# Kernel optimization log

Hardware: AMD Instinct MI355X
Metric: run time of the kernel (lower is better)

Reference implementation:

```python
import jax, jax.numpy as jnp
import numpy as np

DIM, QK, GS, DEPTH, VOCAB, ROT = 16, 128, 256, 8, 1024, 32
EPS = 1e-5


def scale_norm(x, g):
    # ScaleNorm: x / max(||x|| * dim^-0.5, eps) * g
    norm = jnp.linalg.norm(x, axis=-1, keepdims=True) * (DIM ** -0.5)
    return x / jnp.clip(norm, EPS) * g


def rotate_half(x):
    # interleaved pairs: (x0,x1,x2,x3,...) -> (-x1,x0,-x3,x2,...)
    xr = x.reshape(x.shape[:-1] + (-1, 2))
    a, b = xr[..., 0], xr[..., 1]
    return jnp.stack((-b, a), axis=-1).reshape(x.shape)


def apply_rotary(x, cos, sin):
    # rotary applied to first ROT dims only
    xr, xp = x[..., :ROT], x[..., ROT:]
    return jnp.concatenate([xr * cos + rotate_half(xr) * sin, xp], axis=-1)


def flash_layer(x, p, cos, sin, keymask, n):
    b = x.shape[0]
    normed = scale_norm(x, p['norm_g'])
    # shift_tokens: first half of channels shifted forward by one position
    xs, xp = jnp.split(normed, 2, axis=-1)
    xs = jnp.pad(xs, ((0, 0), (1, 0), (0, 0)))[:, :-1]
    normed = jnp.concatenate([xs, xp], axis=-1)
    hid = jax.nn.silu(normed @ p['Wh'] + p['bh'])  # [b,n,64]
    v, gate = jnp.split(hid, 2, axis=-1)           # each [b,n,32]
    qk = jax.nn.silu(normed @ p['Wqk'] + p['bqk'])  # [b,n,128]
    offs = qk[..., None, :] * p['gamma'] + p['beta']  # [b,n,4,128]
    quad_q, lin_q, quad_k, lin_k = [apply_rotary(offs[..., i, :], cos, sin) for i in range(4)]
    pad = (-n) % GS
    grp = lambda t: jnp.pad(t, ((0, 0), (0, pad), (0, 0))).reshape(b, -1, GS, t.shape[-1])
    quad_q, quad_k, lin_q, lin_k, vg = map(grp, (quad_q, quad_k, lin_q, lin_k, v))
    # quadratic (local, within-group) attention with ReLU^2
    sim = jnp.einsum('bgid,bgjd->bgij', quad_q, quad_k) / GS
    attn = jnp.square(jax.nn.relu(sim)) * keymask  # mask out padded keys
    quad_out = jnp.einsum('bgij,bgjd->bgid', attn, vg)
    # linear (global, across-group) attention, reduced over groups
    lin_kv = jnp.einsum('bgnd,bgne->bde', lin_k, vg) / n
    lin_out = jnp.einsum('bgnd,bde->bgne', lin_q, lin_kv)
    out = (quad_out + lin_out).reshape(b, -1, v.shape[-1])[:, :n]
    out = gate * out
    return out @ p['Wo'] + p['bo'] + x


def forward(kmer_data, token_emb, pos_scale, norm_g, Wh, bh, Wqk, bqk, gamma, beta, Wo, bo, final_g, Wl, bl, W1, b1, W2, b2):
    b, n = kmer_data.shape
    x = token_emb[kmer_data]  # [b,n,16]
    t = jnp.arange(n, dtype=jnp.float32)
    # ScaledSinuEmbedding
    inv = 1.0 / (10000.0 ** (jnp.arange(0, DIM, 2, dtype=jnp.float32) / DIM))
    sinu = t[:, None] * inv[None, :]
    pos = jnp.concatenate([jnp.sin(sinu), jnp.cos(sinu)], axis=-1) * pos_scale
    x = x + pos
    # rotary tables (dim 32, interleaved repeat)
    rinv = 1.0 / (10000.0 ** (jnp.arange(0, ROT, 2, dtype=jnp.float32) / ROT))
    rf = jnp.repeat(t[:, None] * rinv[None, :], 2, axis=-1)  # [n,32]
    cos, sin = jnp.cos(rf), jnp.sin(rf)
    # key mask for padded positions (996 -> 1024)
    pad = (-n) % GS
    keymask = jnp.pad(jnp.ones((n,), jnp.float32), (0, pad)).reshape(1, -1, 1, GS)
    for i in range(DEPTH):
        p = dict(norm_g=norm_g[i], Wh=Wh[i], bh=bh[i], Wqk=Wqk[i], bqk=bqk[i],
                 gamma=gamma[i], beta=beta[i], Wo=Wo[i], bo=bo[i])
        x = flash_layer(x, p, cos, sin, keymask, n)
    logits = scale_norm(x, final_g) @ Wl + bl  # [b,n,1024]
    h = jnp.max(logits, axis=-1)               # AdaptiveMaxPool1d(1) + Flatten -> [b,n]
    h = jax.nn.relu(h @ W1 + b1)
    return h @ W2 + b2                          # [b,1]


def setup_inputs() -> dict:
    key = jax.random.key(0)
    ks = jax.random.split(key, 12)
    r = lambda k, shape, s: jax.random.normal(k, shape, jnp.float32) * s
    return {
        'kmer_data': jax.random.randint(ks[0], (128, 996), 0, VOCAB),
        'token_emb': r(ks[1], (VOCAB, DIM), 1.0),
        'pos_scale': jnp.float32(1.0),
        'norm_g': jnp.ones((DEPTH,), jnp.float32),
        'Wh': r(ks[2], (DEPTH, DIM, 64), 0.1),
        'bh': jnp.zeros((DEPTH, 64), jnp.float32),
        'Wqk': r(ks[3], (DEPTH, DIM, QK), 0.1),
        'bqk': jnp.zeros((DEPTH, QK), jnp.float32),
        'gamma': 1.0 + r(ks[4], (DEPTH, 4, QK), 0.02),
        'beta': r(ks[5], (DEPTH, 4, QK), 0.02),
        'Wo': r(ks[6], (DEPTH, 32, DIM), 0.1),
        'bo': jnp.zeros((DEPTH, DIM), jnp.float32),
        'final_g': jnp.float32(1.0),
        'Wl': r(ks[7], (DIM, VOCAB), 0.1),
        'bl': jnp.zeros((VOCAB,), jnp.float32),
        'W1': r(ks[8], (996, 32), 0.05),
        'b1': jnp.zeros((32,), jnp.float32),
        'W2': r(ks[9], (32, 1), 0.1),
        'b2': jnp.zeros((1,), jnp.float32),
    }


def reference(kmer_data, token_emb, pos_scale, norm_g, Wh, bh, Wqk, bqk, gamma, beta, Wo, bo, final_g, Wl, bl, W1, b1, W2, b2):
    return forward(kmer_data, token_emb, pos_scale, norm_g, Wh, bh, Wqk, bqk,
                   gamma, beta, Wo, bo, final_g, Wl, bl, W1, b1, W2, b2)
```

## Files before the change

### kernel.cpp

```cpp
#include <hip/hip_runtime.h>

typedef short s16x8 __attribute__((ext_vector_type(8)));
typedef float f32x4 __attribute__((ext_vector_type(4)));

#define NB    128
#define NTOK  996
#define NPAD  1024
#define NGRP  4
#define GSZ   256
#define NLAY  8

__device__ __forceinline__ float bf2f(unsigned short u){
    unsigned int v = ((unsigned int)u) << 16;
    return __uint_as_float(v);
}
__device__ __forceinline__ unsigned short f2bf(float f){
    unsigned int x = __float_as_uint(f);
    unsigned int r = (x + 0x7fffu + ((x >> 16) & 1u)) >> 16;
    return (unsigned short)r;
}
__device__ __forceinline__ unsigned int packbf(float a, float b){
    return (unsigned int)f2bf(a) | ((unsigned int)f2bf(b) << 16);
}
__device__ __forceinline__ float silu(float v){
    return v / (1.0f + __expf(-v));
}

__device__ __forceinline__ void bar_lds(){
    asm volatile("s_waitcnt lgkmcnt(0)\n\ts_barrier" ::: "memory");
}

__device__ __forceinline__ s16x8 derive_core(const unsigned short* __restrict__ qrow, int d0,
        float4 g0, float4 g1, float4 b0, float4 b1,
        const float* __restrict__ rp, bool rot){
    uint4 u = *(const uint4*)(qrow + d0);
    float y0 = bf2f((unsigned short)(u.x & 0xffffu))*g0.x + b0.x;
    float y1 = bf2f((unsigned short)(u.x >> 16))    *g0.y + b0.y;
    float y2 = bf2f((unsigned short)(u.y & 0xffffu))*g0.z + b0.z;
    float y3 = bf2f((unsigned short)(u.y >> 16))    *g0.w + b0.w;
    float y4 = bf2f((unsigned short)(u.z & 0xffffu))*g1.x + b1.x;
    float y5 = bf2f((unsigned short)(u.z >> 16))    *g1.y + b1.y;
    float y6 = bf2f((unsigned short)(u.w & 0xffffu))*g1.z + b1.z;
    float y7 = bf2f((unsigned short)(u.w >> 16))    *g1.w + b1.w;
    if (rot){
        float4 c4 = *(const float4*)(rp);
        float4 s4 = *(const float4*)(rp + 16);
        float a;
        a = y0; y0 = a*c4.x - y1*s4.x; y1 = y1*c4.x + a*s4.x;
        a = y2; y2 = a*c4.y - y3*s4.y; y3 = y3*c4.y + a*s4.y;
        a = y4; y4 = a*c4.z - y5*s4.z; y5 = y5*c4.z + a*s4.z;
        a = y6; y6 = a*c4.w - y7*s4.w; y7 = y7*c4.w + a*s4.w;
    }
    union { unsigned int uu[4]; s16x8 s; } r;
    r.uu[0] = packbf(y0, y1);
    r.uu[1] = packbf(y2, y3);
    r.uu[2] = packbf(y4, y5);
    r.uu[3] = packbf(y6, y7);
    return r.s;
}

__global__ __launch_bounds__(256) void k_embed(const int* __restrict__ kmer,
                                               const float* __restrict__ emb,
                                               const float* __restrict__ ps,
                                               float* __restrict__ x,
                                               float* __restrict__ rope){
    int gid = blockIdx.x * 256 + threadIdx.x;
    if (gid < NPAD){
        float tf2 = (float)gid;
        #pragma unroll
        for (int i = 0; i < 16; i++){
            float inv = expf(((float)(2*i) / 32.0f) * -9.210340371976184f);
            float ang = tf2 * inv;
            rope[gid*32 + i]      = cosf(ang);
            rope[gid*32 + 16 + i] = sinf(ang);
        }
    }
    if (gid >= NB * NTOK) return;
    int b = gid / NTOK;
    int tt = gid - b * NTOK;
    int idx = kmer[gid];
    const float* er = emb + (size_t)idx * 16;
    float pscale = ps[0];
    float tf = (float)tt;
    float* xr = x + (size_t)gid * 16;
    #pragma unroll
    for (int i = 0; i < 8; i++){
        float inv = expf(((float)(2*i) / 16.0f) * -9.210340371976184f);
        float ang = tf * inv;
        xr[i]     = er[i]     + sinf(ang) * pscale;
        xr[8 + i] = er[8 + i] + cosf(ang) * pscale;
    }
}

__global__ __launch_bounds__(512, 2) void k_pre(const float* __restrict__ x,
                                             const float* __restrict__ Wh, const float* __restrict__ bh,
                                             const float* __restrict__ Wqk, const float* __restrict__ bqk,
                                             const float* __restrict__ norm_g,
                                             const float* __restrict__ gamma, const float* __restrict__ beta,
                                             const float* __restrict__ rope, int layer,
                                             unsigned short* __restrict__ qk,
                                             unsigned short* __restrict__ vT,
                                             unsigned short* __restrict__ gateb,
                                             float* __restrict__ linkvp){
    __shared__ __align__(16) unsigned char sm[58880];
    unsigned short* WcT = (unsigned short*)sm;
    unsigned short* As  = (unsigned short*)(sm + 15360);
    unsigned short* LkT = (unsigned short*)(sm + 15360);
    unsigned short* Vt  = (unsigned short*)(sm + 50176);
    int tid = threadIdx.x;
    int qt = blockIdx.x & 3, b = blockIdx.x >> 2;
    const float* Whl = Wh  + (size_t)layer * 1024;
    const float* Wql = Wqk + (size_t)layer * 2048;
    const float* gLin = gamma + (size_t)layer * 512 + 384;
    const float* bLin = beta  + (size_t)layer * 512 + 384;
    for (int i = tid; i < 1024; i += 512){ int d = i >> 6, c2 = i & 63;  WcT[c2*40 + d] = f2bf(Whl[i]); }
    for (int i = tid; i < 2048; i += 512){ int d = i >> 7, c2 = i & 127; WcT[(64 + c2)*40 + d] = f2bf(Wql[i]); }
    if (tid < 192){
        int i = tid;
        float bv = (i < 64) ? bh[layer*64 + i] : bqk[layer*128 + (i - 64)];
        WcT[i*40 + 16] = f2bf(bv);
        WcT[i*40 + 17] = 0;
        unsigned int* zz = (unsigned int*)(WcT + i*40 + 18);
        #pragma unroll
        for (int k = 0; k < 7; k++) zz[k] = 0u;
    }
    float g = norm_g[layer];
    if (tid < 256){
        int tt = qt*256 + tid;
        int tsafe = tt < NTOK ? tt : (NTOK - 1);
        unsigned int* dd = (unsigned int*)(As + tid * 40);
        const float4* xr4 = (const float4*)(x + ((size_t)b*NTOK + tsafe) * 16);
        float cur[16];
        float s2 = 0.f;
        #pragma unroll
        for (int c2 = 0; c2 < 4; c2++){
            float4 v4 = xr4[c2];
// ... 70 lines not shown
                *(uint2*)(gateb + rowq*32 + (wc0 - 32)) = make_uint2(packbf(sv[0],sv[1]), packbf(sv[2],sv[3]));
            } else {
                int qd = wc0 - 64;
                *(uint2*)(qk + rowq*128 + qd) = make_uint2(packbf(sv[0],sv[1]), packbf(sv[2],sv[3]));
                float y0 = sv[0]*gLin[qd]   + bLin[qd];
                float y1 = sv[1]*gLin[qd+1] + bLin[qd+1];
                float y2 = sv[2]*gLin[qd+2] + bLin[qd+2];
                float y3 = sv[3]*gLin[qd+3] + bLin[qd+3];
                if (qd < 32){
                    const float* rp = rope + ttk*32 + (qd >> 1);
                    float c0 = rp[0], s0 = rp[16], c1 = rp[1], s1 = rp[17];
                    float a;
                    a = y0; y0 = a*c0 - y1*s0; y1 = y1*c0 + a*s0;
                    a = y2; y2 = a*c1 - y3*s1; y3 = y3*c1 + a*s1;
                }
                LkT[(qd+0)*136 + c] = f2bf(y0);
                LkT[(qd+1)*136 + c] = f2bf(y1);
                LkT[(qd+2)*136 + c] = f2bf(y2);
                LkT[(qd+3)*136 + c] = f2bf(y3);
            }
        }
        bar_lds();
        #pragma unroll
        for (int ks2 = 0; ks2 < 4; ks2++){
            s16x8 a  = *(const s16x8*)(LkT + (w*16 + m16)*136 + ks2*32 + quad*8);
            s16x8 b0 = *(const s16x8*)(Vt + (m16)*136 + ks2*32 + quad*8);
            s16x8 b1 = *(const s16x8*)(Vt + (16 + m16)*136 + ks2*32 + quad*8);
            lacc[0] = __builtin_amdgcn_mfma_f32_16x16x32_bf16(a, b0, lacc[0], 0,0,0);
            lacc[1] = __builtin_amdgcn_mfma_f32_16x16x32_bf16(a, b1, lacc[1], 0,0,0);
        }
        bar_lds();
    }
    {
        unsigned short* mv = (unsigned short*)sm + w*1280;
        #pragma unroll
        for (int nt = 0; nt < 2; nt++){
            #pragma unroll
            for (int mi = 0; mi < 2; mi++){
                int e0 = mi*16 + quad*4;
                mv[(e0+0)*40 + nt*16 + m16] = (unsigned short)(vpk[nt][mi][0] & 0xffffu);
                mv[(e0+1)*40 + nt*16 + m16] = (unsigned short)(vpk[nt][mi][0] >> 16);
                mv[(e0+2)*40 + nt*16 + m16] = (unsigned short)(vpk[nt][mi][1] & 0xffffu);
                mv[(e0+3)*40 + nt*16 + m16] = (unsigned short)(vpk[nt][mi][1] >> 16);
            }
        }
        #pragma unroll
        for (int r2 = 0; r2 < 2; r2++){
            int e = r2*16 + (lane >> 2);
            int cc = (lane & 3) * 8;
            s16x8 vv = *(const s16x8*)(mv + e*40 + cc);
            *(s16x8*)(vT + ((size_t)b*32 + e)*NPAD + qt*256 + w*32 + cc) = vv;
        }
    }
    {
        float* ml = (float*)(sm + 20480) + w*512;
        const float invn = 1.0f / 996.0f;
        #pragma unroll
        for (int j = 0; j < 2; j++)
            #pragma unroll
            for (int reg = 0; reg < 4; reg++)
                ml[(j*16 + m16)*16 + quad*4 + reg] = lacc[j][reg] * invn;
        #pragma unroll
        for (int r2 = 0; r2 < 2; r2++){
            int e = r2*16 + (lane >> 2);
            int dc = (lane & 3) * 4;
            float4 vv = *(const float4*)(ml + e*16 + dc);
            *(float4*)(linkvp + (((size_t)qt*NB + b)*32 + e)*128 + w*16 + dc) = vv;
        }
    }
}

#define KD_BYTES (64*136*2)
#define PW_BYTES (8*32*72*2)
__global__ __launch_bounds__(512, 2) void k_quad(const unsigned short* __restrict__ qk,
                                              const unsigned short* __restrict__ vT,
                                              const unsigned short* __restrict__ gateb,
                                              const float* __restrict__ linkvp,
                                              const float* __restrict__ rope,
                                              const float* __restrict__ gamma, const float* __restrict__ beta,
                                              int layer,
                                              const float* __restrict__ Wo, const float* __restrict__ bo,
                                              float* __restrict__ x){
    __shared__ __align__(16) unsigned char smem[KD_BYTES + PW_BYTES];
    __shared__ __align__(16) unsigned short LkBs[32 * 136];
    __shared__ float sWo[512];
    __shared__ float sbo[16];
    unsigned short* Kd = (unsigned short*)smem;
    unsigned short* Pw = (unsigned short*)(smem + KD_BYTES);
    int tid = threadIdx.x;
    int blk = blockIdx.x;
    int g = blk & 3, b = blk >> 2;
    int tg0 = g * GSZ;
    const float* gamL = gamma + (size_t)layer * 512;
    const float* betL = beta  + (size_t)layer * 512;
    sWo[tid] = Wo[layer*512 + tid];
    if (tid < 16) sbo[tid] = bo[layer*16 + tid];

    int w = tid >> 6, lane = tid & 63, m16 = lane & 15, quad = lane >> 4;

    int tqA = tg0 + w*32 + m16;
    int tqB = tqA + 16;
    const unsigned short* qrowA = qk + ((size_t)b*NPAD + tqA)*128;
    const unsigned short* qrowB = qk + ((size_t)b*NPAD + tqB)*128;
    const float* rpA = rope + tqA*32 + quad*4;
    const float* rpB = rope + tqB*32 + quad*4;
    s16x8 qf[2][4];
    #pragma unroll
    for (int ks = 0; ks < 4; ks++){
        int d0 = ks*32 + quad*8;
        float4 g0 = *(const float4*)(gamL + d0), g1 = *(const float4*)(gamL + d0 + 4);
        float4 b0 = *(const float4*)(betL + d0), b1 = *(const float4*)(betL + d0 + 4);
        bool rot = (ks == 0) && (quad < 4);
        qf[0][ks] = derive_core(qrowA, d0, g0,g1,b0,b1, rpA, rot);
        qf[1][ks] = derive_core(qrowB, d0, g0,g1,b0,b1, rpB, rot);
    }

    const float* gK = gamL + 256;
    const float* bK = betL + 256;
    f32x4 oacc[2][2] = {{{0,0,0,0},{0,0,0,0}},{{0,0,0,0},{0,0,0,0}}};
    unsigned short* myP = Pw + w*32*72;

    int kr = tid >> 3, seg = (tid & 7) * 16;
    uint4 pku0, pku1;
    float4 prc0, prc1, prs0, prs1;
    auto LOADK = [&](int ch){
        int tk = tg0 + ch*64 + kr;
        const unsigned short* krow = qk + ((size_t)b*NPAD + tk)*128 + seg;
        pku0 = ((const uint4*)krow)[0];
        pku1 = ((const uint4*)krow)[1];
        const float* rpk = rope + (seg < 32 ? (tk*32 + (seg >> 1)) : 0);
        prc0 = *(const float4*)(rpk);
        prs0 = *(const float4*)(rpk + 16);
        prc1 = *(const float4*)(rpk + 4);
        prs1 = *(const float4*)(rpk + 20);
    };
    LOADK(0);

    for (int ch = 0; ch < 4; ch++){
        s16x8 vf[2][2];
        #pragma unroll
        for (int ks2 = 0; ks2 < 2; ks2++){
            vf[ks2][0] = *(const s16x8*)(vT + ((size_t)b*32 + m16)*NPAD + tg0 + ch*64 + ks2*32 + quad*8);
            vf[ks2][1] = *(const s16x8*)(vT + ((size_t)b*32 + 16 + m16)*NPAD + tg0 + ch*64 + ks2*32 + quad*8);
        }
        uint4 kd0, kd1;
        {
            #pragma unroll
            for (int h = 0; h < 2; h++){
                uint4 u = h ? pku1 : pku0;
                unsigned int uu[4] = {u.x, u.y, u.z, u.w};
                float y[8];
                #pragma unroll
                for (int k = 0; k < 4; k++){
                    int d = h*8 + 2*k;
                    y[2*k]   = bf2f((unsigned short)(uu[k] & 0xffffu)) * gK[seg + d]     + bK[seg + d];
                    y[2*k+1] = bf2f((unsigned short)(uu[k] >> 16))     * gK[seg + d + 1] + bK[seg + d + 1];
                }
                if (seg < 32){
                    float cc[4], ss[4];
                    if (h){ cc[0]=prc1.x; cc[1]=prc1.y; cc[2]=prc1.z; cc[3]=prc1.w;
                            ss[0]=prs1.x; ss[1]=prs1.y; ss[2]=prs1.z; ss[3]=prs1.w; }
                    else  { cc[0]=prc0.x; cc[1]=prc0.y; cc[2]=prc0.z; cc[3]=prc0.w;
                            ss[0]=prs0.x; ss[1]=prs0.y; ss[2]=prs0.z; ss[3]=prs0.w; }
                    #pragma unroll
                    for (int p2 = 0; p2 < 4; p2++){
                        float a = y[2*p2], d2 = y[2*p2+1];
                        y[2*p2]   = a*cc[p2] - d2*ss[p2];
                        y[2*p2+1] = d2*cc[p2] + a*ss[p2];
                    }
                }
                uint4 kk = make_uint4(packbf(y[0],y[1]), packbf(y[2],y[3]),
                                      packbf(y[4],y[5]), packbf(y[6],y[7]));
                if (h) kd1 = kk; else kd0 = kk;
            }
        }
        bar_lds();
        *(uint4*)(Kd + kr*136 + seg)     = kd0;
        *(uint4*)(Kd + kr*136 + seg + 8) = kd1;
        if (ch < 3) LOADK(ch + 1);
        bar_lds();
        #pragma unroll
        for (int np = 0; np < 2; np++){
            f32x4 s00 = {0,0,0,0}, s01 = {0,0,0,0}, s10 = {0,0,0,0}, s11 = {0,0,0,0};
            #pragma unroll
            for (int ks = 0; ks < 4; ks++){
                s16x8 kf0 = *(const s16x8*)(Kd + ((np*2  )*16 + m16)*136 + ks*32 + quad*8);
                s16x8 kf1 = *(const s16x8*)(Kd + ((np*2+1)*16 + m16)*136 + ks*32 + quad*8);
                s00 = __builtin_amdgcn_mfma_f32_16x16x32_bf16(qf[0][ks], kf0, s00, 0,0,0);
                s01 = __builtin_amdgcn_mfma_f32_16x16x32_bf16(qf[0][ks], kf1, s01, 0,0,0);
                s10 = __builtin_amdgcn_mfma_f32_16x16x32_bf16(qf[1][ks], kf0, s10, 0,0,0);
                s11 = __builtin_amdgcn_mfma_f32_16x16x32_bf16(qf[1][ks], kf1, s11, 0,0,0);
            }
            #pragma unroll
            for (int j = 0; j < 2; j++){
                int kl = (np*2 + j)*16 + m16;
                bool kv = (tg0 + ch*64 + kl) < NTOK;
                #pragma unroll
                for (int reg = 0; reg < 4; reg++){
                    float a0 = fmaxf(j ? s01[reg] : s00[reg], 0.0f);
                    float a1 = fmaxf(j ? s11[reg] : s10[reg], 0.0f);
                    a0 = a0 * a0;
                    a1 = a1 * a1;
                    myP[(quad*4 + reg)*72 + kl]      = kv ? f2bf(a0) : (unsigned short)0;
                    myP[(16 + quad*4 + reg)*72 + kl] = kv ? f2bf(a1) : (unsigned short)0;
                }
            }
        }
        #pragma unroll
        for (int i = 0; i < 2; i++){
            #pragma unroll
            for (int ks2 = 0; ks2 < 2; ks2++){
                s16x8 pa = *(const s16x8*)(myP + (i*16 + m16)*72 + ks2*32 + quad*8);
                oacc[i][0] = __builtin_amdgcn_mfma_f32_16x16x32_bf16(pa, vf[ks2][0], oacc[i][0], 0,0,0);
                oacc[i][1] = __builtin_amdgcn_mfma_f32_16x16x32_bf16(pa, vf[ks2][1], oacc[i][1], 0,0,0);
            }
        }
    }
    const float qsc = 1.0f / 65536.0f;
    #pragma unroll
    for (int i = 0; i < 2; i++)
        #pragma unroll
        for (int j = 0; j < 2; j++)
            oacc[i][j] = oacc[i][j] * qsc;
    {
        int e = tid >> 4, dbase = (tid & 15) * 8;
        float s[8];
        #pragma unroll
        for (int k = 0; k < 8; k++) s[k] = 0.f;
        #pragma unroll
        for (int part = 0; part < 4; part++){
            const float* src = linkvp + (((size_t)part*NB + b)*32 + e)*128 + dbase;
            float4 u0 = *(const float4*)src;
            float4 u1 = *(const float4*)(src + 4);
            s[0]+=u0.x; s[1]+=u0.y; s[2]+=u0.z; s[3]+=u0.w;
            s[4]+=u1.x; s[5]+=u1.y; s[6]+=u1.z; s[7]+=u1.w;
        }
        unsigned int* dst = (unsigned int*)(LkBs + e*136 + dbase);
        #pragma unroll
        for (int k = 0; k < 4; k++) dst[k] = packbf(s[2*k], s[2*k+1]);
    }
    bar_lds();
    int pr = lane >> 1, dp2 = (lane & 1) * 8;
    int p = tg0 + w*32 + pr;
    bool pvld = p < NTOK;
    int psafe = pvld ? p : (NTOK - 1);
    const unsigned short* gr = gateb + ((size_t)b*NPAD + psafe)*32;
    uint4 egu[4];
    #pragma unroll
    for (int eh = 0; eh < 4; eh++) egu[eh] = *(const uint4*)(gr + eh*8);
    float* xr = x + ((size_t)b*NTOK + psafe)*16 + dp2;
    float4 ex0 = *(const float4*)xr;
    float4 ex1 = *(const float4*)(xr + 4);
    {
        const float* gamQ = gamL + 128;
        const float* betQ = betL + 128;
        #pragma unroll
        for (int ks = 0; ks < 4; ks++){
            int d0 = ks*32 + quad*8;
            float4 g0 = *(const float4*)(gamQ + d0), g1 = *(const float4*)(gamQ + d0 + 4);
            float4 b0 = *(const float4*)(betQ + d0), b1 = *(const float4*)(betQ + d0 + 4);
            bool rot = (ks == 0) && (quad < 4);
            s16x8 lf0 = derive_core(qrowA, d0, g0,g1,b0,b1, rpA, rot);
            s16x8 lf1 = derive_core(qrowB, d0, g0,g1,b0,b1, rpB, rot);
            #pragma unroll
            for (int j = 0; j < 2; j++){
                s16x8 lb = *(const s16x8*)(LkBs + (j*16 + m16)*136 + ks*32 + quad*8);
                oacc[0][j] = __builtin_amdgcn_mfma_f32_16x16x32_bf16(lf0, lb, oacc[0][j], 0,0,0);
                oacc[1][j] = __builtin_amdgcn_mfma_f32_16x16x32_bf16(lf1, lb, oacc[1][j], 0,0,0);
            }
        }
    }
    float* Obw = (float*)smem + w*1056;
    #pragma unroll
    for (int i = 0; i < 2; i++)
        #pragma unroll
        for (int j = 0; j < 2; j++)
            #pragma unroll
            for (int reg = 0; reg < 4; reg++)
                Obw[(i*16 + quad*4 + reg)*33 + j*16 + m16] = oacc[i][j][reg];
    if (pvld){
        float a[8] = { sbo[dp2]+ex0.x, sbo[dp2+1]+ex0.y, sbo[dp2+2]+ex0.z, sbo[dp2+3]+ex0.w,
                       sbo[dp2+4]+ex1.x, sbo[dp2+5]+ex1.y, sbo[dp2+6]+ex1.z, sbo[dp2+7]+ex1.w };
        #pragma unroll
        for (int eh = 0; eh < 4; eh++){
            unsigned int gg[4] = {egu[eh].x, egu[eh].y, egu[eh].z, egu[eh].w};
            #pragma unroll
            for (int k = 0; k < 4; k++){
                float gv0 = bf2f((unsigned short)(gg[k] & 0xffffu));
                float gv1 = bf2f((unsigned short)(gg[k] >> 16));
                int e = eh*8 + 2*k;
                float ov0 = Obw[pr*33 + e] * gv0;
                float ov1 = Obw[pr*33 + e + 1] * gv1;
                const float* wr0 = &sWo[e*16 + dp2];
                const float* wr1 = &sWo[(e+1)*16 + dp2];
                #pragma unroll
                for (int kk = 0; kk < 8; kk++) a[kk] += ov0 * wr0[kk] + ov1 * wr1[kk];
            }
        }
        *(float4*)xr = make_float4(a[0],a[1],a[2],a[3]);
        *(float4*)(xr+4) = make_float4(a[4],a[5],a[6],a[7]);
    }
}

__global__ __launch_bounds__(256) void k_head(const float* __restrict__ x,
                                              const float* __restrict__ Wl, const float* __restrict__ bl,
                                              const float* __restrict__ fg, float* __restrict__ h){
    __shared__ __align__(16) unsigned short WlT[512 * 40];
    __shared__ __align__(16) unsigned short As[256 * 40];
    int tid = threadIdx.x;
    int gid0 = blockIdx.x * 256;
    {
        int t = gid0 + tid;
        const float4* xr4 = (const float4*)(x + (size_t)t * 16);
        float cur[16]; float s2 = 0.f;
        #pragma unroll
        for (int c = 0; c < 4; c++){
            float4 v4 = xr4[c];
            cur[4*c] = v4.x; cur[4*c+1] = v4.y; cur[4*c+2] = v4.z; cur[4*c+3] = v4.w;
        }
        #pragma unroll
        for (int d = 0; d < 16; d++) s2 += cur[d]*cur[d];
        float sc = fg[0] / fmaxf(sqrtf(s2) * 0.25f, 1e-5f);
        unsigned int* dd = (unsigned int*)(As + tid * 40);
        #pragma unroll
        for (int i = 0; i < 8; i++) dd[i] = packbf(cur[2*i]*sc, cur[2*i+1]*sc);
        dd[8] = 0x00003f80u;
        #pragma unroll
// ... 81 lines not shown
        out[b] = s;
    }
}

extern "C" void kernel_launch(void* const* d_in, const int* in_sizes, int n_in,
                              void* d_out, int out_size, void* d_ws, size_t ws_size,
                              hipStream_t stream){
    const int*   kmer  = (const int*)d_in[0];
    const float* emb   = (const float*)d_in[1];
    const float* ps    = (const float*)d_in[2];
    const float* ng    = (const float*)d_in[3];
    const float* Wh    = (const float*)d_in[4];
    const float* bh    = (const float*)d_in[5];
    const float* Wqk   = (const float*)d_in[6];
    const float* bqk   = (const float*)d_in[7];
    const float* gamma = (const float*)d_in[8];
    const float* beta  = (const float*)d_in[9];
    const float* Wo    = (const float*)d_in[10];
    const float* bo    = (const float*)d_in[11];
    const float* fg    = (const float*)d_in[12];
    const float* Wl    = (const float*)d_in[13];
    const float* bl    = (const float*)d_in[14];
    const float* W1    = (const float*)d_in[15];
    const float* b1    = (const float*)d_in[16];
    const float* W2    = (const float*)d_in[17];
    const float* b2    = (const float*)d_in[18];
    float* out = (float*)d_out;

    char* wsp = (char*)d_ws;
    float* x = (float*)wsp;                     wsp += (size_t)NB*NTOK*16*4;
    unsigned short* qk = (unsigned short*)wsp;  wsp += (size_t)NB*NPAD*128*2;
    unsigned short* vT = (unsigned short*)wsp;  wsp += (size_t)NB*32*NPAD*2;
    unsigned short* gateb = (unsigned short*)wsp; wsp += (size_t)NB*NPAD*32*2;
    float* linkvp = (float*)wsp;                wsp += (size_t)4*NB*32*128*4;
    float* rope = (float*)wsp;                  wsp += (size_t)NPAD*32*4;
    float* h = (float*)wsp;                     wsp += (size_t)NB*NTOK*4;

    k_embed<<<(NB*NTOK + 255)/256, 256, 0, stream>>>(kmer, emb, ps, x, rope);
    for (int layer = 0; layer < NLAY; layer++){
        k_pre<<<NB*4, 512, 0, stream>>>(x, Wh, bh, Wqk, bqk, ng, gamma, beta, rope, layer, qk, vT, gateb, linkvp);
        k_quad<<<NB*NGRP, 512, 0, stream>>>(qk, vT, gateb, linkvp, rope, gamma, beta, layer, Wo, bo, x);
    }
    k_head<<<NB*NTOK/256, 256, 0, stream>>>(x, Wl, bl, fg, h);
    k_final<<<NB, 256, 0, stream>>>(h, W1, b1, W2, b2, out);
}
```

Baseline: 750.5 us.

## Double-buffer K tiles in k_quad and reduce linear KV via atomics

k_quad now keeps two shared-memory K buffers. The next chunk's K is derived and stored between the two score halves, which removes one barrier per chunk and overlaps global loads with MFMA work. The P tile is shrunk to 32 columns, and the score-to-output MFMAs are interleaved per half. k_pre now atomically adds its linear KV partials into a single per-batch buffer, replacing the four partial copies that k_quad summed. That buffer alternates between layers, and k_quad zeroes the other copy for the next layer. This trades a partial-sum read pass for atomic traffic and adds ordering dependencies between kernels.

```diff
diff --git a/kernel.cpp b/kernel.cpp
--- a/kernel.cpp
+++ b/kernel.cpp
@@ -9,6 +9,7 @@
 #define NGRP  4
 #define GSZ   256
 #define NLAY  8
+#define LKV_FLOATS (NB*32*128)
 
 __device__ __forceinline__ float bf2f(unsigned short u){
     unsigned int v = ((unsigned int)u) << 16;
@@ -63,8 +64,11 @@
                                                const float* __restrict__ emb,
                                                const float* __restrict__ ps,
                                                float* __restrict__ x,
-                                               float* __restrict__ rope){
+                                               float* __restrict__ rope,
+                                               float* __restrict__ linkv0){
     int gid = blockIdx.x * 256 + threadIdx.x;
+    for (int i = gid; i < LKV_FLOATS/4; i += 127488)
+        *(float4*)(linkv0 + (size_t)i*4) = make_float4(0.f,0.f,0.f,0.f);
     if (gid < NPAD){
         float tf2 = (float)gid;
         #pragma unroll
@@ -101,7 +105,7 @@
                                              unsigned short* __restrict__ qk,
                                              unsigned short* __restrict__ vT,
                                              unsigned short* __restrict__ gateb,
-                                             float* __restrict__ linkvp){
+                                             float* __restrict__ linkv){
     __shared__ __align__(16) unsigned char sm[58880];
     unsigned short* WcT = (unsigned short*)sm;
     unsigned short* As  = (unsigned short*)(sm + 15360);
@@ -238,6 +242,19 @@
         bar_lds();
     }
     {
+        const float invn = 1.0f / 996.0f;
+        float* dstb = linkv + (size_t)b*32*128;
+        #pragma unroll
+        for (int j = 0; j < 2; j++){
+            int e = j*16 + m16;
+            #pragma unroll
+            for (int reg = 0; reg < 4; reg++){
+                int d = w*16 + quad*4 + reg;
+                atomicAdd(dstb + (size_t)e*128 + d, lacc[j][reg] * invn);
+            }
+        }
+    }
+    {
         unsigned short* mv = (unsigned short*)sm + w*1280;
         #pragma unroll
         for (int nt = 0; nt < 2; nt++){
@@ -258,73 +275,38 @@
             *(s16x8*)(vT + ((size_t)b*32 + e)*NPAD + qt*256 + w*32 + cc) = vv;
         }
     }
-    {
-        float* ml = (float*)(sm + 20480) + w*512;
-        const float invn = 1.0f / 996.0f;
-        #pragma unroll
-        for (int j = 0; j < 2; j++)
-            #pragma unroll
-            for (int reg = 0; reg < 4; reg++)
-                ml[(j*16 + m16)*16 + quad*4 + reg] = lacc[j][reg] * invn;
-        #pragma unroll
-        for (int r2 = 0; r2 < 2; r2++){
-            int e = r2*16 + (lane >> 2);
-            int dc = (lane & 3) * 4;
-            float4 vv = *(const float4*)(ml + e*16 + dc);
-            *(float4*)(linkvp + (((size_t)qt*NB + b)*32 + e)*128 + w*16 + dc) = vv;
-        }
-    }
-}
-
-#define KD_BYTES (64*136*2)
-#define PW_BYTES (8*32*72*2)
+}
+
+#define KD_SH   8704
+#define KD2_BYTES (2*64*136*2)
+#define PW_BYTES  (8*32*40*2)
 __global__ __launch_bounds__(512, 2) void k_quad(const unsigned short* __restrict__ qk,
                                               const unsigned short* __restrict__ vT,
                                               const unsigned short* __restrict__ gateb,
-                                              const float* __restrict__ linkvp,
+                                              const float* __restrict__ linkv,
+                                              float* __restrict__ lkz,
                                               const float* __restrict__ rope,
                                               const float* __restrict__ gamma, const float* __restrict__ beta,
                                               int layer,
                                               const float* __restrict__ Wo, const float* __restrict__ bo,
                                               float* __restrict__ x){
-    __shared__ __align__(16) unsigned char smem[KD_BYTES + PW_BYTES];
-    __shared__ __align__(16) unsigned short LkBs[32 * 136];
+    __shared__ __align__(16) unsigned char smem[KD2_BYTES + PW_BYTES];
     __shared__ float sWo[512];
     __shared__ float sbo[16];
-    unsigned short* Kd = (unsigned short*)smem;
-    unsigned short* Pw = (unsigned short*)(smem + KD_BYTES);
+    unsigned short* Kd   = (unsigned short*)smem;
+    unsigned short* Pw   = (unsigned short*)(smem + KD2_BYTES);
+    unsigned short* LkBs = (unsigned short*)(smem + KD2_BYTES);
     int tid = threadIdx.x;
     int blk = blockIdx.x;
     int g = blk & 3, b = blk >> 2;
     int tg0 = g * GSZ;
+    *(float2*)(lkz + (size_t)blk*1024 + tid*2) = make_float2(0.f, 0.f);
     const float* gamL = gamma + (size_t)layer * 512;
     const float* betL = beta  + (size_t)layer * 512;
     sWo[tid] = Wo[layer*512 + tid];
     if (tid < 16) sbo[tid] = bo[layer*16 + tid];
 
     int w = tid >> 6, lane = tid & 63, m16 = lane & 15, quad = lane >> 4;
-
-    int tqA = tg0 + w*32 + m16;
-    int tqB = tqA + 16;
-    const unsigned short* qrowA = qk + ((size_t)b*NPAD + tqA)*128;
-    const unsigned short* qrowB = qk + ((size_t)b*NPAD + tqB)*128;
-    const float* rpA = rope + tqA*32 + quad*4;
-    const float* rpB = rope + tqB*32 + quad*4;
-    s16x8 qf[2][4];
-    #pragma unroll
-    for (int ks = 0; ks < 4; ks++){
-        int d0 = ks*32 + quad*8;
-        float4 g0 = *(const float4*)(gamL + d0), g1 = *(const float4*)(gamL + d0 + 4);
-        float4 b0 = *(const float4*)(betL + d0), b1 = *(const float4*)(betL + d0 + 4);
-        bool rot = (ks == 0) && (quad < 4);
-        qf[0][ks] = derive_core(qrowA, d0, g0,g1,b0,b1, rpA, rot);
-        qf[1][ks] = derive_core(qrowB, d0, g0,g1,b0,b1, rpB, rot);
-    }
-
-    const float* gK = gamL + 256;
-    const float* bK = betL + 256;
-    f32x4 oacc[2][2] = {{{0,0,0,0},{0,0,0,0}},{{0,0,0,0},{0,0,0,0}}};
-    unsigned short* myP = Pw + w*32*72;
 
     int kr = tid >> 3, seg = (tid & 7) * 16;
     uint4 pku0, pku1;
@@ -334,64 +316,99 @@
         const unsigned short* krow = qk + ((size_t)b*NPAD + tk)*128 + seg;
         pku0 = ((const uint4*)krow)[0];
         pku1 = ((const uint4*)krow)[1];
-        const float* rpk = rope + (seg < 32 ? (tk*32 + (seg >> 1)) : 0);
-        prc0 = *(const float4*)(rpk);
-        prs0 = *(const float4*)(rpk + 16);
-        prc1 = *(const float4*)(rpk + 4);
-        prs1 = *(const float4*)(rpk + 20);
+        if (seg < 32){
+            const float* rpk = rope + tk*32 + (seg >> 1);
+            prc0 = *(const float4*)(rpk);
+            prs0 = *(const float4*)(rpk + 16);
+            prc1 = *(const float4*)(rpk + 4);
+            prs1 = *(const float4*)(rpk + 20);
+        }
     };
+    const float* gK = gamL + 256;
+    const float* bK = betL + 256;
+    auto DERIVEK = [&](uint4& kd0, uint4& kd1){
+        #pragma unroll
+        for (int h = 0; h < 2; h++){
+            uint4 u = h ? pku1 : pku0;
+            unsigned int uu[4] = {u.x, u.y, u.z, u.w};
+            float y[8];
+            #pragma unroll
+            for (int k = 0; k < 4; k++){
+                int d = h*8 + 2*k;
+                y[2*k]   = bf2f((unsigned short)(uu[k] & 0xffffu)) * gK[seg + d]     + bK[seg + d];
+                y[2*k+1] = bf2f((unsigned short)(uu[k] >> 16))     * gK[seg + d + 1] + bK[seg + d + 1];
+            }
+            if (seg < 32){
+                float cc[4], ss[4];
+                if (h){ cc[0]=prc1.x; cc[1]=prc1.y; cc[2]=prc1.z; cc[3]=prc1.w;
+                        ss[0]=prs1.x; ss[1]=prs1.y; ss[2]=prs1.z; ss[3]=prs1.w; }
+                else  { cc[0]=prc0.x; cc[1]=prc0.y; cc[2]=prc0.z; cc[3]=prc0.w;
+                        ss[0]=prs0.x; ss[1]=prs0.y; ss[2]=prs0.z; ss[3]=prs0.w; }
+                #pragma unroll
+                for (int p2 = 0; p2 < 4; p2++){
+                    float a = y[2*p2], d2 = y[2*p2+1];
+                    y[2*p2]   = a*cc[p2] - d2*ss[p2];
+                    y[2*p2+1] = d2*cc[p2] + a*ss[p2];
+                }
+            }
+            uint4 kk = make_uint4(packbf(y[0],y[1]), packbf(y[2],y[3]),
+                                  packbf(y[4],y[5]), packbf(y[6],y[7]));
+            if (h) kd1 = kk; else kd0 = kk;
+        }
+    };
+
     LOADK(0);
 
+    int tqA = tg0 + w*32 + m16;
+    int tqB = tqA + 16;
+    const unsigned short* qrowA = qk + ((size_t)b*NPAD + tqA)*128;
+    const unsigned short* qrowB = qk + ((size_t)b*NPAD + tqB)*128;
+    const float* rpA = rope + tqA*32 + quad*4;
+    const float* rpB = rope + tqB*32 + quad*4;
+    s16x8 qf[2][4];
+    #pragma unroll
+    for (int ks = 0; ks < 4; ks++){
+        int d0 = ks*32 + quad*8;
+        float4 g0 = *(const float4*)(gamL + d0), g1 = *(const float4*)(gamL + d0 + 4);
+        float4 b0 = *(const float4*)(betL + d0), b1 = *(const float4*)(betL + d0 + 4);
+        bool rot = (ks == 0) && (quad < 4);
+        qf[0][ks] = derive_core(qrowA, d0, g0,g1,b0,b1, rpA, rot);
+        qf[1][ks] = derive_core(qrowB, d0, g0,g1,b0,b1, rpB, rot);
+    }
+
+    {
+        uint4 kd0, kd1;
+        DERIVEK(kd0, kd1);
+        *(uint4*)(Kd + kr*136 + seg)     = kd0;
+        *(uint4*)(Kd + kr*136 + seg + 8) = kd1;
+    }
+    LOADK(1);
+
+    f32x4 oacc[2][2] = {{{0,0,0,0},{0,0,0,0}},{{0,0,0,0},{0,0,0,0}}};
+    unsigned short* myP = Pw + w*1280;
+    float4 lkvA, lkvB;
+
     for (int ch = 0; ch < 4; ch++){
+        bar_lds();
         s16x8 vf[2][2];
         #pragma unroll
         for (int ks2 = 0; ks2 < 2; ks2++){
             vf[ks2][0] = *(const s16x8*)(vT + ((size_t)b*32 + m16)*NPAD + tg0 + ch*64 + ks2*32 + quad*8);
             vf[ks2][1] = *(const s16x8*)(vT + ((size_t)b*32 + 16 + m16)*NPAD + tg0 + ch*64 + ks2*32 + quad*8);
         }
-        uint4 kd0, kd1;
-        {
-            #pragma unroll
-            for (int h = 0; h < 2; h++){
-                uint4 u = h ? pku1 : pku0;
-                unsigned int uu[4] = {u.x, u.y, u.z, u.w};
-                float y[8];
-                #pragma unroll
-                for (int k = 0; k < 4; k++){
-                    int d = h*8 + 2*k;
-                    y[2*k]   = bf2f((unsigned short)(uu[k] & 0xffffu)) * gK[seg + d]     + bK[seg + d];
-                    y[2*k+1] = bf2f((unsigned short)(uu[k] >> 16))     * gK[seg + d + 1] + bK[seg + d + 1];
-                }
-                if (seg < 32){
-                    float cc[4], ss[4];
-                    if (h){ cc[0]=prc1.x; cc[1]=prc1.y; cc[2]=prc1.z; cc[3]=prc1.w;
-                            ss[0]=prs1.x; ss[1]=prs1.y; ss[2]=prs1.z; ss[3]=prs1.w; }
-                    else  { cc[0]=prc0.x; cc[1]=prc0.y; cc[2]=prc0.z; cc[3]=prc0.w;
-                            ss[0]=prs0.x; ss[1]=prs0.y; ss[2]=prs0.z; ss[3]=prs0.w; }
-                    #pragma unroll
-                    for (int p2 = 0; p2 < 4; p2++){
-                        float a = y[2*p2], d2 = y[2*p2+1];
-                        y[2*p2]   = a*cc[p2] - d2*ss[p2];
-                        y[2*p2+1] = d2*cc[p2] + a*ss[p2];
-                    }
-                }
-                uint4 kk = make_uint4(packbf(y[0],y[1]), packbf(y[2],y[3]),
-                                      packbf(y[4],y[5]), packbf(y[6],y[7]));
-                if (h) kd1 = kk; else kd0 = kk;
-            }
-        }
-        bar_lds();
-        *(uint4*)(Kd + kr*136 + seg)     = kd0;
-        *(uint4*)(Kd + kr*136 + seg + 8) = kd1;
-        if (ch < 3) LOADK(ch + 1);
-        bar_lds();
+        if (ch == 3){
+            const float* src = linkv + ((size_t)b*32 + (tid >> 4))*128 + (tid & 15)*8;
+            lkvA = *(const float4*)src;
+            lkvB = *(const float4*)(src + 4);
+        }
+        unsigned short* Kc = Kd + (ch & 1)*KD_SH;
         #pragma unroll
         for (int np = 0; np < 2; np++){
             f32x4 s00 = {0,0,0,0}, s01 = {0,0,0,0}, s10 = {0,0,0,0}, s11 = {0,0,0,0};
             #pragma unroll
             for (int ks = 0; ks < 4; ks++){
-                s16x8 kf0 = *(const s16x8*)(Kd + ((np*2  )*16 + m16)*136 + ks*32 + quad*8);
-                s16x8 kf1 = *(const s16x8*)(Kd + ((np*2+1)*16 + m16)*136 + ks*32 + quad*8);
+                s16x8 kf0 = *(const s16x8*)(Kc + ((np*2  )*16 + m16)*136 + ks*32 + quad*8);
+                s16x8 kf1 = *(const s16x8*)(Kc + ((np*2+1)*16 + m16)*136 + ks*32 + quad*8);
                 s00 = __builtin_amdgcn_mfma_f32_16x16x32_bf16(qf[0][ks], kf0, s00, 0,0,0);
                 s01 = __builtin_amdgcn_mfma_f32_16x16x32_bf16(qf[0][ks], kf1, s01, 0,0,0);
                 s10 = __builtin_amdgcn_mfma_f32_16x16x32_bf16(qf[1][ks], kf0, s10, 0,0,0);
@@ -399,26 +416,31 @@
             }
             #pragma unroll
             for (int j = 0; j < 2; j++){
-                int kl = (np*2 + j)*16 + m16;
-                bool kv = (tg0 + ch*64 + kl) < NTOK;
+                int kl = j*16 + m16;
+                bool kv = (tg0 + ch*64 + np*32 + kl) < NTOK;
                 #pragma unroll
                 for (int reg = 0; reg < 4; reg++){
                     float a0 = fmaxf(j ? s01[reg] : s00[reg], 0.0f);
                     float a1 = fmaxf(j ? s11[reg] : s10[reg], 0.0f);
                     a0 = a0 * a0;
                     a1 = a1 * a1;
-                    myP[(quad*4 + reg)*72 + kl]      = kv ? f2bf(a0) : (unsigned short)0;
-                    myP[(16 + quad*4 + reg)*72 + kl] = kv ? f2bf(a1) : (unsigned short)0;
+                    myP[(quad*4 + reg)*40 + kl]      = kv ? f2bf(a0) : (unsigned short)0;
+                    myP[(16 + quad*4 + reg)*40 + kl] = kv ? f2bf(a1) : (unsigned short)0;
                 }
             }
-        }
-        #pragma unroll
-        for (int i = 0; i < 2; i++){
-            #pragma unroll
-            for (int ks2 = 0; ks2 < 2; ks2++){
-                s16x8 pa = *(const s16x8*)(myP + (i*16 + m16)*72 + ks2*32 + quad*8);
-                oacc[i][0] = __builtin_amdgcn_mfma_f32_16x16x32_bf16(pa, vf[ks2][0], oacc[i][0], 0,0,0);
-                oacc[i][1] = __builtin_amdgcn_mfma_f32_16x16x32_bf16(pa, vf[ks2][1], oacc[i][1], 0,0,0);
+            #pragma unroll
+            for (int i = 0; i < 2; i++){
+                s16x8 pa = *(const s16x8*)(myP + (i*16 + m16)*40 + quad*8);
+                oacc[i][0] = __builtin_amdgcn_mfma_f32_16x16x32_bf16(pa, vf[np][0], oacc[i][0], 0,0,0);
+                oacc[i][1] = __builtin_amdgcn_mfma_f32_16x16x32_bf16(pa, vf[np][1], oacc[i][1], 0,0,0);
+            }
+            if (np == 0 && ch < 3){
+                uint4 kd0, kd1;
+                DERIVEK(kd0, kd1);
+                unsigned short* Kn = Kd + ((ch+1) & 1)*KD_SH;
+                *(uint4*)(Kn + kr*136 + seg)     = kd0;
+                *(uint4*)(Kn + kr*136 + seg + 8) = kd1;
+                if (ch < 2) LOADK(ch + 2);
             }
         }
     }
@@ -428,22 +450,14 @@
         #pragma unroll
         for (int j = 0; j < 2; j++)
             oacc[i][j] = oacc[i][j] * qsc;
+    bar_lds();
     {
-        int e = tid >> 4, dbase = (tid & 15) * 8;
-        float s[8];
-        #pragma unroll
-        for (int k = 0; k < 8; k++) s[k] = 0.f;
-        #pragma unroll
-        for (int part = 0; part < 4; part++){
-            const float* src = linkvp + (((size_t)part*NB + b)*32 + e)*128 + dbase;
-            float4 u0 = *(const float4*)src;
-            float4 u1 = *(const float4*)(src + 4);
-            s[0]+=u0.x; s[1]+=u0.y; s[2]+=u0.z; s[3]+=u0.w;
-            s[4]+=u1.x; s[5]+=u1.y; s[6]+=u1.z; s[7]+=u1.w;
-        }
+        int e = tid >> 4, dbase = (tid & 15)*8;
         unsigned int* dst = (unsigned int*)(LkBs + e*136 + dbase);
-        #pragma unroll
-        for (int k = 0; k < 4; k++) dst[k] = packbf(s[2*k], s[2*k+1]);
+        dst[0] = packbf(lkvA.x, lkvA.y);
+        dst[1] = packbf(lkvA.z, lkvA.w);
+        dst[2] = packbf(lkvB.x, lkvB.y);
+        dst[3] = packbf(lkvB.z, lkvB.w);
     }
     bar_lds();
     int pr = lane >> 1, dp2 = (lane & 1) * 8;
@@ -646,14 +660,16 @@
     unsigned short* qk = (unsigned short*)wsp;  wsp += (size_t)NB*NPAD*128*2;
     unsigned short* vT = (unsigned short*)wsp;  wsp += (size_t)NB*32*NPAD*2;
     unsigned short* gateb = (unsigned short*)wsp; wsp += (size_t)NB*NPAD*32*2;
-    float* linkvp = (float*)wsp;                wsp += (size_t)4*NB*32*128*4;
+    float* linkv = (float*)wsp;                 wsp += (size_t)2*LKV_FLOATS*4;
     float* rope = (float*)wsp;                  wsp += (size_t)NPAD*32*4;
     float* h = (float*)wsp;                     wsp += (size_t)NB*NTOK*4;
 
-    k_embed<<<(NB*NTOK + 255)/256, 256, 0, stream>>>(kmer, emb, ps, x, rope);
+    k_embed<<<(NB*NTOK + 255)/256, 256, 0, stream>>>(kmer, emb, ps, x, rope, linkv);
     for (int layer = 0; layer < NLAY; layer++){
-        k_pre<<<NB*4, 512, 0, stream>>>(x, Wh, bh, Wqk, bqk, ng, gamma, beta, rope, layer, qk, vT, gateb, linkvp);
-        k_quad<<<NB*NGRP, 512, 0, stream>>>(qk, vT, gateb, linkvp, rope, gamma, beta, layer, Wo, bo, x);
+        float* lkA = linkv + (size_t)(layer & 1)*LKV_FLOATS;
+        float* lkZ = linkv + (size_t)((layer + 1) & 1)*LKV_FLOATS;
+        k_pre<<<NB*4, 512, 0, stream>>>(x, Wh, bh, Wqk, bqk, ng, gamma, beta, rope, layer, qk, vT, gateb, lkA);
+        k_quad<<<NB*NGRP, 512, 0, stream>>>(qk, vT, gateb, lkA, lkZ, rope, gamma, beta, layer, Wo, bo, x);
     }
     k_head<<<NB*NTOK/256, 256, 0, stream>>>(x, Wl, bl, fg, h);
     k_final<<<NB, 256, 0, stream>>>(h, W1, b1, W2, b2, out);
```

Measured after the change: 905.4 us. +20.6%, slower.

## Double-buffer K tiles and interleave P·V per half-chunk in quad attention

Applied to the files above, without the earlier changes.

Converts the K-tile staging in k_quad to a two-buffer LDS ping-pong. The next chunk's K derivation and store, plus the global prefetch of the chunk after it, now run between the two score half-steps, which leaves one barrier per chunk instead of two. V fragments are prefetched one chunk ahead in registers, and the P buffer shrinks to a 32-column half-chunk so P·V runs right after each half's scores. The linkvp loads are hoisted ahead of a barrier, and LkBs now aliases the P buffer. The cost is more registers (two V fragment sets) and more LDS for the second K buffer, which could threaten the 2-blocks-per-CU launch bound.

```diff
diff --git a/kernel.cpp b/kernel.cpp
--- a/kernel.cpp
+++ b/kernel.cpp
@@ -276,8 +276,9 @@
     }
 }
 
-#define KD_BYTES (64*136*2)
-#define PW_BYTES (8*32*72*2)
+#define KD_SH   8704
+#define KD2_BYTES (2*64*136*2)
+#define PW_BYTES  (8*32*40*2)
 __global__ __launch_bounds__(512, 2) void k_quad(const unsigned short* __restrict__ qk,
                                               const unsigned short* __restrict__ vT,
                                               const unsigned short* __restrict__ gateb,
@@ -287,12 +288,12 @@
                                               int layer,
                                               const float* __restrict__ Wo, const float* __restrict__ bo,
                                               float* __restrict__ x){
-    __shared__ __align__(16) unsigned char smem[KD_BYTES + PW_BYTES];
-    __shared__ __align__(16) unsigned short LkBs[32 * 136];
+    __shared__ __align__(16) unsigned char smem[KD2_BYTES + PW_BYTES];
     __shared__ float sWo[512];
     __shared__ float sbo[16];
-    unsigned short* Kd = (unsigned short*)smem;
-    unsigned short* Pw = (unsigned short*)(smem + KD_BYTES);
+    unsigned short* Kd   = (unsigned short*)smem;
+    unsigned short* Pw   = (unsigned short*)(smem + KD2_BYTES);
+    unsigned short* LkBs = (unsigned short*)(smem + KD2_BYTES);
     int tid = threadIdx.x;
     int blk = blockIdx.x;
     int g = blk & 3, b = blk >> 2;
@@ -304,28 +305,6 @@
 
     int w = tid >> 6, lane = tid & 63, m16 = lane & 15, quad = lane >> 4;
 
-    int tqA = tg0 + w*32 + m16;
-    int tqB = tqA + 16;
-    const unsigned short* qrowA = qk + ((size_t)b*NPAD + tqA)*128;
-    const unsigned short* qrowB = qk + ((size_t)b*NPAD + tqB)*128;
-    const float* rpA = rope + tqA*32 + quad*4;
-    const float* rpB = rope + tqB*32 + quad*4;
-    s16x8 qf[2][4];
-    #pragma unroll
-    for (int ks = 0; ks < 4; ks++){
-        int d0 = ks*32 + quad*8;
-        float4 g0 = *(const float4*)(gamL + d0), g1 = *(const float4*)(gamL + d0 + 4);
-        float4 b0 = *(const float4*)(betL + d0), b1 = *(const float4*)(betL + d0 + 4);
-        bool rot = (ks == 0) && (quad < 4);
-        qf[0][ks] = derive_core(qrowA, d0, g0,g1,b0,b1, rpA, rot);
-        qf[1][ks] = derive_core(qrowB, d0, g0,g1,b0,b1, rpB, rot);
-    }
-
-    const float* gK = gamL + 256;
-    const float* bK = betL + 256;
-    f32x4 oacc[2][2] = {{{0,0,0,0},{0,0,0,0}},{{0,0,0,0},{0,0,0,0}}};
-    unsigned short* myP = Pw + w*32*72;
-
     int kr = tid >> 3, seg = (tid & 7) * 16;
     uint4 pku0, pku1;
     float4 prc0, prc1, prs0, prs1;
@@ -334,64 +313,99 @@
         const unsigned short* krow = qk + ((size_t)b*NPAD + tk)*128 + seg;
         pku0 = ((const uint4*)krow)[0];
         pku1 = ((const uint4*)krow)[1];
-        const float* rpk = rope + (seg < 32 ? (tk*32 + (seg >> 1)) : 0);
-        prc0 = *(const float4*)(rpk);
-        prs0 = *(const float4*)(rpk + 16);
-        prc1 = *(const float4*)(rpk + 4);
-        prs1 = *(const float4*)(rpk + 20);
+        if (seg < 32){
+            const float* rpk = rope + tk*32 + (seg >> 1);
+            prc0 = *(const float4*)(rpk);
+            prs0 = *(const float4*)(rpk + 16);
+            prc1 = *(const float4*)(rpk + 4);
+            prs1 = *(const float4*)(rpk + 20);
+        }
     };
-    LOADK(0);
-
-    for (int ch = 0; ch < 4; ch++){
-        s16x8 vf[2][2];
+    const float* gK = gamL + 256;
+    const float* bK = betL + 256;
+    auto DERIVEK = [&](uint4& kd0, uint4& kd1){
+        #pragma unroll
+        for (int h = 0; h < 2; h++){
+            uint4 u = h ? pku1 : pku0;
+            unsigned int uu[4] = {u.x, u.y, u.z, u.w};
+            float y[8];
+            #pragma unroll
+            for (int k = 0; k < 4; k++){
+                int d = h*8 + 2*k;
+                y[2*k]   = bf2f((unsigned short)(uu[k] & 0xffffu)) * gK[seg + d]     + bK[seg + d];
+                y[2*k+1] = bf2f((unsigned short)(uu[k] >> 16))     * gK[seg + d + 1] + bK[seg + d + 1];
+            }
+            if (seg < 32){
+                float cc[4], ss[4];
+                if (h){ cc[0]=prc1.x; cc[1]=prc1.y; cc[2]=prc1.z; cc[3]=prc1.w;
+                        ss[0]=prs1.x; ss[1]=prs1.y; ss[2]=prs1.z; ss[3]=prs1.w; }
+                else  { cc[0]=prc0.x; cc[1]=prc0.y; cc[2]=prc0.z; cc[3]=prc0.w;
+                        ss[0]=prs0.x; ss[1]=prs0.y; ss[2]=prs0.z; ss[3]=prs0.w; }
+                #pragma unroll
+                for (int p2 = 0; p2 < 4; p2++){
+                    float a = y[2*p2], d2 = y[2*p2+1];
+                    y[2*p2]   = a*cc[p2] - d2*ss[p2];
+                    y[2*p2+1] = d2*cc[p2] + a*ss[p2];
+                }
+            }
+            uint4 kk = make_uint4(packbf(y[0],y[1]), packbf(y[2],y[3]),
+                                  packbf(y[4],y[5]), packbf(y[6],y[7]));
+            if (h) kd1 = kk; else kd0 = kk;
+        }
+    };
+    auto LOADV = [&](int ch, s16x8 vf[2][2]){
         #pragma unroll
         for (int ks2 = 0; ks2 < 2; ks2++){
             vf[ks2][0] = *(const s16x8*)(vT + ((size_t)b*32 + m16)*NPAD + tg0 + ch*64 + ks2*32 + quad*8);
             vf[ks2][1] = *(const s16x8*)(vT + ((size_t)b*32 + 16 + m16)*NPAD + tg0 + ch*64 + ks2*32 + quad*8);
         }
+    };
+
+    LOADK(0);
+
+    int tqA = tg0 + w*32 + m16;
+    int tqB = tqA + 16;
+    const unsigned short* qrowA = qk + ((size_t)b*NPAD + tqA)*128;
+    const unsigned short* qrowB = qk + ((size_t)b*NPAD + tqB)*128;
+    const float* rpA = rope + tqA*32 + quad*4;
+    const float* rpB = rope + tqB*32 + quad*4;
+    s16x8 qf[2][4];
+    #pragma unroll
+    for (int ks = 0; ks < 4; ks++){
+        int d0 = ks*32 + quad*8;
+        float4 g0 = *(const float4*)(gamL + d0), g1 = *(const float4*)(gamL + d0 + 4);
+        float4 b0 = *(const float4*)(betL + d0), b1 = *(const float4*)(betL + d0 + 4);
+        bool rot = (ks == 0) && (quad < 4);
+        qf[0][ks] = derive_core(qrowA, d0, g0,g1,b0,b1, rpA, rot);
+        qf[1][ks] = derive_core(qrowB, d0, g0,g1,b0,b1, rpB, rot);
+    }
+
+    {
         uint4 kd0, kd1;
-        {
-            #pragma unroll
-            for (int h = 0; h < 2; h++){
-                uint4 u = h ? pku1 : pku0;
-                unsigned int uu[4] = {u.x, u.y, u.z, u.w};
-                float y[8];
-                #pragma unroll
-                for (int k = 0; k < 4; k++){
-                    int d = h*8 + 2*k;
-                    y[2*k]   = bf2f((unsigned short)(uu[k] & 0xffffu)) * gK[seg + d]     + bK[seg + d];
-                    y[2*k+1] = bf2f((unsigned short)(uu[k] >> 16))     * gK[seg + d + 1] + bK[seg + d + 1];
-                }
-                if (seg < 32){
-                    float cc[4], ss[4];
-                    if (h){ cc[0]=prc1.x; cc[1]=prc1.y; cc[2]=prc1.z; cc[3]=prc1.w;
-                            ss[0]=prs1.x; ss[1]=prs1.y; ss[2]=prs1.z; ss[3]=prs1.w; }
-                    else  { cc[0]=prc0.x; cc[1]=prc0.y; cc[2]=prc0.z; cc[3]=prc0.w;
-                            ss[0]=prs0.x; ss[1]=prs0.y; ss[2]=prs0.z; ss[3]=prs0.w; }
-                    #pragma unroll
-                    for (int p2 = 0; p2 < 4; p2++){
-                        float a = y[2*p2], d2 = y[2*p2+1];
-                        y[2*p2]   = a*cc[p2] - d2*ss[p2];
-                        y[2*p2+1] = d2*cc[p2] + a*ss[p2];
-                    }
-                }
-                uint4 kk = make_uint4(packbf(y[0],y[1]), packbf(y[2],y[3]),
-                                      packbf(y[4],y[5]), packbf(y[6],y[7]));
-                if (h) kd1 = kk; else kd0 = kk;
-            }
-        }
-        bar_lds();
+        DERIVEK(kd0, kd1);
         *(uint4*)(Kd + kr*136 + seg)     = kd0;
         *(uint4*)(Kd + kr*136 + seg + 8) = kd1;
-        if (ch < 3) LOADK(ch + 1);
+    }
+    LOADK(1);
+    s16x8 vfA[2][2];
+    LOADV(0, vfA);
+
+    f32x4 oacc[2][2] = {{{0,0,0,0},{0,0,0,0}},{{0,0,0,0},{0,0,0,0}}};
+    unsigned short* myP = Pw + w*1280;
+
+    #pragma unroll
+    for (int ch = 0; ch < 4; ch++){
         bar_lds();
+        s16x8 vfB[2][2];
+        if (ch < 3) LOADV(ch + 1, vfB);
+        unsigned short* Kc = Kd + (ch & 1)*KD_SH;
         #pragma unroll
         for (int np = 0; np < 2; np++){
             f32x4 s00 = {0,0,0,0}, s01 = {0,0,0,0}, s10 = {0,0,0,0}, s11 = {0,0,0,0};
             #pragma unroll
             for (int ks = 0; ks < 4; ks++){
-                s16x8 kf0 = *(const s16x8*)(Kd + ((np*2  )*16 + m16)*136 + ks*32 + quad*8);
-                s16x8 kf1 = *(const s16x8*)(Kd + ((np*2+1)*16 + m16)*136 + ks*32 + quad*8);
+                s16x8 kf0 = *(const s16x8*)(Kc + ((np*2  )*16 + m16)*136 + ks*32 + quad*8);
+                s16x8 kf1 = *(const s16x8*)(Kc + ((np*2+1)*16 + m16)*136 + ks*32 + quad*8);
                 s00 = __builtin_amdgcn_mfma_f32_16x16x32_bf16(qf[0][ks], kf0, s00, 0,0,0);
                 s01 = __builtin_amdgcn_mfma_f32_16x16x32_bf16(qf[0][ks], kf1, s01, 0,0,0);
                 s10 = __builtin_amdgcn_mfma_f32_16x16x32_bf16(qf[1][ks], kf0, s10, 0,0,0);
@@ -399,26 +413,38 @@
             }
             #pragma unroll
             for (int j = 0; j < 2; j++){
-                int kl = (np*2 + j)*16 + m16;
-                bool kv = (tg0 + ch*64 + kl) < NTOK;
+                int kl = j*16 + m16;
+                bool kv = (tg0 + ch*64 + np*32 + kl) < NTOK;
                 #pragma unroll
                 for (int reg = 0; reg < 4; reg++){
                     float a0 = fmaxf(j ? s01[reg] : s00[reg], 0.0f);
                     float a1 = fmaxf(j ? s11[reg] : s10[reg], 0.0f);
                     a0 = a0 * a0;
                     a1 = a1 * a1;
-                    myP[(quad*4 + reg)*72 + kl]      = kv ? f2bf(a0) : (unsigned short)0;
-                    myP[(16 + quad*4 + reg)*72 + kl] = kv ? f2bf(a1) : (unsigned short)0;
+                    myP[(quad*4 + reg)*40 + kl]      = kv ? f2bf(a0) : (unsigned short)0;
+                    myP[(16 + quad*4 + reg)*40 + kl] = kv ? f2bf(a1) : (unsigned short)0;
                 }
             }
-        }
-        #pragma unroll
-        for (int i = 0; i < 2; i++){
+            #pragma unroll
+            for (int i = 0; i < 2; i++){
+                s16x8 pa = *(const s16x8*)(myP + (i*16 + m16)*40 + quad*8);
+                oacc[i][0] = __builtin_amdgcn_mfma_f32_16x16x32_bf16(pa, vfA[np][0], oacc[i][0], 0,0,0);
+                oacc[i][1] = __builtin_amdgcn_mfma_f32_16x16x32_bf16(pa, vfA[np][1], oacc[i][1], 0,0,0);
+            }
+            if (np == 0 && ch < 3){
+                uint4 kd0, kd1;
+                DERIVEK(kd0, kd1);
+                unsigned short* Kn = Kd + ((ch+1) & 1)*KD_SH;
+                *(uint4*)(Kn + kr*136 + seg)     = kd0;
+                *(uint4*)(Kn + kr*136 + seg + 8) = kd1;
+                if (ch < 2) LOADK(ch + 2);
+            }
+        }
+        if (ch < 3){
             #pragma unroll
             for (int ks2 = 0; ks2 < 2; ks2++){
-                s16x8 pa = *(const s16x8*)(myP + (i*16 + m16)*72 + ks2*32 + quad*8);
-                oacc[i][0] = __builtin_amdgcn_mfma_f32_16x16x32_bf16(pa, vf[ks2][0], oacc[i][0], 0,0,0);
-                oacc[i][1] = __builtin_amdgcn_mfma_f32_16x16x32_bf16(pa, vf[ks2][1], oacc[i][1], 0,0,0);
+                vfA[ks2][0] = vfB[ks2][0];
+                vfA[ks2][1] = vfB[ks2][1];
             }
         }
     }
@@ -428,18 +454,23 @@
         #pragma unroll
         for (int j = 0; j < 2; j++)
             oacc[i][j] = oacc[i][j] * qsc;
+    int e = tid >> 4, dbase = (tid & 15) * 8;
+    float4 lp[4][2];
+    #pragma unroll
+    for (int part = 0; part < 4; part++){
+        const float* src = linkvp + (((size_t)part*NB + b)*32 + e)*128 + dbase;
+        lp[part][0] = *(const float4*)src;
+        lp[part][1] = *(const float4*)(src + 4);
+    }
+    bar_lds();
     {
-        int e = tid >> 4, dbase = (tid & 15) * 8;
         float s[8];
         #pragma unroll
         for (int k = 0; k < 8; k++) s[k] = 0.f;
         #pragma unroll
         for (int part = 0; part < 4; part++){
-            const float* src = linkvp + (((size_t)part*NB + b)*32 + e)*128 + dbase;
-            float4 u0 = *(const float4*)src;
-            float4 u1 = *(const float4*)(src + 4);
-            s[0]+=u0.x; s[1]+=u0.y; s[2]+=u0.z; s[3]+=u0.w;
-            s[4]+=u1.x; s[5]+=u1.y; s[6]+=u1.z; s[7]+=u1.w;
+            s[0]+=lp[part][0].x; s[1]+=lp[part][0].y; s[2]+=lp[part][0].z; s[3]+=lp[part][0].w;
+            s[4]+=lp[part][1].x; s[5]+=lp[part][1].y; s[6]+=lp[part][1].z; s[7]+=lp[part][1].w;
         }
         unsigned int* dst = (unsigned int*)(LkBs + e*136 + dbase);
         #pragma unroll
@@ -494,11 +525,11 @@
             for (int k = 0; k < 4; k++){
                 float gv0 = bf2f((unsigned short)(gg[k] & 0xffffu));
                 float gv1 = bf2f((unsigned short)(gg[k] >> 16));
-                int e = eh*8 + 2*k;
-                float ov0 = Obw[pr*33 + e] * gv0;
-                float ov1 = Obw[pr*33 + e + 1] * gv1;
-                const float* wr0 = &sWo[e*16 + dp2];
-                const float* wr1 = &sWo[(e+1)*16 + dp2];
+                int ee = eh*8 + 2*k;
+                float ov0 = Obw[pr*33 + ee] * gv0;
+                float ov1 = Obw[pr*33 + ee + 1] * gv1;
+                const float* wr0 = &sWo[ee*16 + dp2];
+                const float* wr1 = &sWo[(ee+1)*16 + dp2];
                 #pragma unroll
                 for (int kk = 0; kk < 8; kk++) a[kk] += ov0 * wr0[kk] + ov1 * wr1[kk];
             }
```

After: 758.3 us. About the same (+1.0%).
